# Performance work log

Measured on AMD Instinct MI355X. Metric: run time of the kernel, lower is better.

The kernel has to match this reference:

```python
import jax, jax.numpy as jnp
import numpy as np

EMBED_DIM = 512
Q_DIM = 64
V_DIM = 64
WINDOW_SIZE = 128
B, N = 2, 4096


def setup_inputs() -> dict:
    key = jax.random.key(0)
    ks = jax.random.split(key, 7)
    s = 1.0 / np.sqrt(EMBED_DIM)
    u = lambda k, shape: jax.random.uniform(k, shape, jnp.float32, -s, s)
    return {
        "x": jax.random.normal(ks[0], (B, N, EMBED_DIM), jnp.float32),
        "Wq": u(ks[1], (EMBED_DIM, Q_DIM)),
        "bq": u(ks[2], (Q_DIM,)),
        "Wk": u(ks[3], (EMBED_DIM, Q_DIM)),
        "bk": u(ks[4], (Q_DIM,)),
        "Wv": u(ks[5], (EMBED_DIM, V_DIM)),
        "bv": u(ks[6], (V_DIM,)),
    }


def reference(x, Wq, bq, Wk, bk, Wv, bv):
    b, n, _ = x.shape
    w = WINDOW_SIZE // 2
    Q = x @ Wq + bq  # (b, n, Qd)
    K = x @ Wk + bk  # (b, n, Qd)
    V = x @ Wv + bv  # (b, n, Vd)

    diags = jnp.arange(-w, w + 1)            # (nd,) offsets di
    nd = diags.shape[0]
    # Gather K[i + di] via padded K; invalid positions masked to 0 afterwards.
    Kpad = jnp.pad(K, ((0, 0), (w, w), (0, 0)))
    j = jnp.arange(n)[:, None] + diags[None, :]          # (n, nd) = i + di
    Kg = Kpad[:, j + w, :]                               # (b, n, nd, Qd)
    scores = jnp.einsum('bnd,bnod->bno', Q, Kg)          # (b, n, nd)
    valid = (j >= 0) & (j < n)
    scores = jnp.where(valid[None], scores, 0.0)

    # Faithful to original: diagonal dot products are scattered into the FIRST
    # nd columns of a dense (b, n, n) matrix (rest zeros), softmax over the
    # full n columns, then dense matmul with V.
    columns = jnp.zeros((b, n, n), dtype=x.dtype).at[:, :, :nd].set(scores)
    attn = jax.nn.softmax(columns, axis=2)               # (b, n, n)
    return attn @ V                                      # (b, n, Vd)
```

## Files before the change

### kernel.cpp

```cpp
#include <hip/hip_runtime.h>

typedef short short8 __attribute__((ext_vector_type(8)));
typedef float f32x4 __attribute__((ext_vector_type(4)));

#define NN 4096
#define NE 512
#define HD 64
#define KROWS 4288
#define KOFF  64

__device__ __forceinline__ unsigned short bf_trunc(float f) {
    union { float f; unsigned u; } c; c.f = f;
    return (unsigned short)(c.u >> 16);
}
__device__ __forceinline__ void bf_split(float f, unsigned short& hi, unsigned short& lo) {
    union { float f; unsigned u; } c; c.f = f;
    unsigned uh = c.u & 0xFFFF0000u;
    hi = (unsigned short)(uh >> 16);
    union { float f; unsigned u; } d; d.u = uh;
    lo = bf_trunc(f - d.f);
}

#define MFMA16(a, b, c) __builtin_amdgcn_mfma_f32_16x16x32_bf16((a), (b), (c), 0, 0, 0)

__global__ __launch_bounds__(256) void wprep_kernel(
    const float* __restrict__ Wq, const float* __restrict__ Wk,
    const float* __restrict__ Wv,
    unsigned short* __restrict__ Wfhi, unsigned short* __restrict__ Wflo,
    unsigned short* __restrict__ Khi, unsigned short* __restrict__ Klo,
    unsigned short* __restrict__ Vfhi, unsigned short* __restrict__ Vflo,
    float* __restrict__ Vs)
{
    const int gtid = blockIdx.x * 256 + threadIdx.x;
    const int L = gtid & 63;
    {
        const int nt = (gtid >> 6) % 12;
        const int kt = gtid / 768;
        const int n = nt * 16 + (L & 15);
        const int kbase = kt * 32 + (L >> 4) * 8;
        const float* src; int col;
        if (n < 64)       { src = Wq; col = n; }
        else if (n < 128) { src = Wk; col = n - 64; }
        else              { src = Wv; col = n - 128; }
        short8 sh, sl;
#pragma unroll
        for (int j = 0; j < 8; ++j) {
            unsigned short h, l;
            bf_split(src[(size_t)(kbase + j) * HD + col], h, l);
            sh[j] = (short)h; sl[j] = (short)l;
        }
        *(short8*)(Wfhi + (size_t)gtid * 8) = sh;
        *(short8*)(Wflo + (size_t)gtid * 8) = sl;
    }
    if (gtid < 6144) {
        const int p = gtid >> 3, o = gtid & 7;
        const int b = p / 192, q = p - b * 192;
        const size_t row = (size_t)b * KROWS + (q < 64 ? q : 4096 + q);
        const short8 z = {0, 0, 0, 0, 0, 0, 0, 0};
        *(short8*)(Khi + row * HD + o * 8) = z;
        *(short8*)(Klo + row * HD + o * 8) = z;
    }
    if (gtid < 3200) {
        const int rem = gtid % 1600;
        const int jt = rem / 320;
        const int nt = (rem / 64) % 5;
        short8 sh = {0, 0, 0, 0, 0, 0, 0, 0};
        const short8 z = {0, 0, 0, 0, 0, 0, 0, 0};
        if (nt == 4 && (L & 15) == 0) {
#pragma unroll
            for (int jj = 0; jj < 8; ++jj) {
                const int j = jt * 32 + (L >> 4) * 8 + jj;
                if (j < 129) sh[jj] = (short)0x3F80;
            }
        }
        *(short8*)(Vfhi + (size_t)gtid * 8) = sh;
        *(short8*)(Vflo + (size_t)gtid * 8) = z;
    }
    if (gtid < 128) Vs[gtid] = 0.f;
}

__global__ __launch_bounds__(256, 2) void proj_kernel(
    const float* __restrict__ x,
    const unsigned short* __restrict__ Wfhi, const unsigned short* __restrict__ Wflo,
    const float* __restrict__ bq, const float* __restrict__ bk,
    const float* __restrict__ bv,
    unsigned short* __restrict__ Qhi, unsigned short* __restrict__ Qlo,
    unsigned short* __restrict__ Khi, unsigned short* __restrict__ Klo,
    unsigned short* __restrict__ Vfhi, unsigned short* __restrict__ Vflo,
    float* __restrict__ Vs)
{
    __shared__ float V_lds[16][68];
    const int tid = threadIdx.x;
    const int L = tid & 63;
    const int w = tid >> 6;
    const int m = L & 15, kg = L >> 4;
    const int blk = blockIdx.x;
    const int r0 = blk * 16;
    const int b = blk >> 8;

    const float* xp = x + (size_t)(r0 + m) * NE + kg * 8;
    const unsigned short* wfh = Wfhi + (size_t)(w * 3) * 512 + L * 8;
    const unsigned short* wfl = Wflo + (size_t)(w * 3) * 512 + L * 8;

    f32x4 acc[3];
#pragma unroll
    for (int t = 0; t < 3; ++t) acc[t] = (f32x4){0.f, 0.f, 0.f, 0.f};

    float4 cx0[3], cx1[3];
    short8 cwh[3][3], cwl[3][3];

#pragma unroll
    for (int p = 0; p < 2; ++p) {
        cx0[p] = *(const float4*)(xp + p * 32);
        cx1[p] = *(const float4*)(xp + p * 32 + 4);
#pragma unroll
        for (int t = 0; t < 3; ++t) {
            cwh[p][t] = *(const short8*)(wfh + (size_t)p * 6144 + t * 512);
            cwl[p][t] = *(const short8*)(wfl + (size_t)p * 6144 + t * 512);
        }
    }

#pragma unroll
    for (int kt = 0; kt < 16; ++kt) {
        const int cur = kt % 3;
        const int nxt = (kt + 2) % 3;
        if (kt + 2 < 16) {
            cx0[nxt] = *(const float4*)(xp + (kt + 2) * 32);
            cx1[nxt] = *(const float4*)(xp + (kt + 2) * 32 + 4);
#pragma unroll
            for (int t = 0; t < 3; ++t) {
                cwh[nxt][t] = *(const short8*)(wfh + (size_t)(kt + 2) * 6144 + t * 512);
                cwl[nxt][t] = *(const short8*)(wfl + (size_t)(kt + 2) * 6144 + t * 512);
            }
        }
        const float xv[8] = {cx0[cur].x, cx0[cur].y, cx0[cur].z, cx0[cur].w,
                             cx1[cur].x, cx1[cur].y, cx1[cur].z, cx1[cur].w};
        short8 ahi, alo;
#pragma unroll
        for (int j = 0; j < 8; ++j) {
            unsigned short h, l; bf_split(xv[j], h, l);
            ahi[j] = (short)h; alo[j] = (short)l;
        }
#pragma unroll
        for (int t = 0; t < 3; ++t) {
            acc[t] = MFMA16(ahi, cwh[cur][t], acc[t]);
            acc[t] = MFMA16(alo, cwh[cur][t], acc[t]);
            acc[t] = MFMA16(ahi, cwl[cur][t], acc[t]);
        }
    }

#pragma unroll
    for (int t = 0; t < 3; ++t) {
        const int nt = w * 3 + t;
        const int cgc = nt * 16 + m;
        const float bias = (cgc < 64) ? bq[cgc]
                         : (cgc < 128) ? bk[cgc - 64] : bv[cgc - 128];
#pragma unroll
        for (int r = 0; r < 4; ++r) {
            const int gr = r0 + kg * 4 + r;
            const float val = acc[t][r] + bias;
            if (cgc < 64) {
                unsigned short h, l; bf_split(val, h, l);
                Qhi[(size_t)gr * HD + cgc] = h;
                Qlo[(size_t)gr * HD + cgc] = l;
            } else if (cgc < 128) {
                const int d = cgc - 64, n = gr & 4095;
                const size_t idx = ((size_t)b * KROWS + KOFF + n) * HD + d;
                unsigned short h, l; bf_split(val, h, l);
                Khi[idx] = h; Klo[idx] = l;
            } else {
                V_lds[kg * 4 + r][cgc - 128] = val;
            }
        }
    }
    __syncthreads();

    if (tid < 64) {
        float s = 0.f;
#pragma unroll
        for (int r = 0; r < 16; ++r) s += V_lds[r][tid];
        atomicAdd(&Vs[b * HD + tid], s);
    }

    if ((blk & 255) <= 8) {
        const int n0v = r0 & 4095;
        const int jt = n0v >> 5;
        const int h = (n0v >> 4) & 1;
        if ((kg >> 1) == h) {
            const int nt = w;
            short8 sh, sl;
#pragma unroll
            for (int jj = 0; jj < 8; ++jj) {
                const int j = jt * 32 + kg * 8 + jj;
                float val = 0.f;
                if (j < 129) val = V_lds[j - n0v][nt * 16 + m];
                unsigned short hh, ll; bf_split(val, hh, ll);
                sh[jj] = (short)hh; sl[jj] = (short)ll;
            }
            const size_t fo = ((size_t)((b * 25 + jt * 5 + nt) * 64 + L)) * 8;
            *(short8*)(Vfhi + fo) = sh;
            *(short8*)(Vflo + fo) = sl;
        }
    }
}

__global__ __launch_bounds__(256) void attn_kernel(
    const unsigned short* __restrict__ Qhi, const unsigned short* __restrict__ Qlo,
    const unsigned short* __restrict__ Khi, const unsigned short* __restrict__ Klo,
    const unsigned short* __restrict__ Vfhi, const unsigned short* __restrict__ Vflo,
    const float* __restrict__ Vs, float* __restrict__ out)
{
    __shared__ __align__(16) unsigned short wt_hi[16 * 168];
    __shared__ __align__(16) unsigned short wt_lo[16 * 168];
    __shared__ float den_lds[16];

    const int tid = threadIdx.x;
    const int L = tid & 63;
    const int w = tid >> 6;
    const int m = L & 15, kg = L >> 4;
    const int b = blockIdx.x >> 8;
    const int n0 = (blockIdx.x & 255) * 16;

    const unsigned short* qp  = Qhi + ((size_t)(b * NN + n0 + m)) * HD + kg * 8;
    const unsigned short* qp2 = Qlo + ((size_t)(b * NN + n0 + m)) * HD + kg * 8;
    const short8 qhi0 = *(const short8*)(qp);
    const short8 qhi1 = *(const short8*)(qp + 32);
    const short8 qlo0 = *(const short8*)(qp2);
    const short8 qlo1 = *(const short8*)(qp2 + 32);

    int kts[3]; int nkt;
    if (w == 3) { kts[0] = 3; kts[1] = 7; kts[2] = 8; nkt = 3; }
    else        { kts[0] = w; kts[1] = w + 4; kts[2] = 0; nkt = 2; }

    const unsigned short* KB  = Khi + (size_t)b * KROWS * HD;
    const unsigned short* KB2 = Klo + (size_t)b * KROWS * HD;
    short8 kh0[3], kh1[3], kl0[3], kl1[3];
#pragma unroll
    for (int i = 0; i < 3; ++i) {
        if (i < nkt) {
            const size_t krow = (size_t)(n0 + kts[i] * 16 + m);
            const unsigned short* kp  = KB  + krow * HD + kg * 8;
            const unsigned short* kp2 = KB2 + krow * HD + kg * 8;
            kh0[i] = *(const short8*)(kp);
            kh1[i] = *(const short8*)(kp + 32);
            kl0[i] = *(const short8*)(kp2);
            kl1[i] = *(const short8*)(kp2 + 32);
        }
    }

    short8 vhi[5], vlo[5], vh4[5];
#pragma unroll
    for (int jt = 0; jt < 5; ++jt) {
        const size_t fo = ((size_t)((b * 25 + jt * 5 + w) * 64 + L)) * 8;
        vhi[jt] = *(const short8*)(Vfhi + fo);
        vlo[jt] = *(const short8*)(Vflo + fo);
    }
    if (w == 0) {
#pragma unroll
        for (int jt = 0; jt < 5; ++jt) {
            const size_t fo4 = ((size_t)((b * 25 + jt * 5 + 4) * 64 + L)) * 8;
            vh4[jt] = *(const short8*)(Vfhi + fo4);
        }
    }

    for (int i = tid; i < (16 * 168) / 2; i += 256) {
        ((int*)wt_hi)[i] = 0;
        ((int*)wt_lo)[i] = 0;
    }
    __syncthreads();

#pragma unroll
    for (int i = 0; i < 3; ++i) {
        if (i < nkt) {
            f32x4 acc = (f32x4){0.f, 0.f, 0.f, 0.f};
            acc = MFMA16(qhi0, kh0[i], acc);
            acc = MFMA16(qhi1, kh1[i], acc);
            acc = MFMA16(qlo0, kh0[i], acc);
            acc = MFMA16(qlo1, kh1[i], acc);
            acc = MFMA16(qhi0, kl0[i], acc);
            acc = MFMA16(qhi1, kl1[i], acc);
            const int l = kts[i] * 16 + m;
#pragma unroll
            for (int r = 0; r < 4; ++r) {
                const int q = kg * 4 + r;
                const int j = l - q;
                if (j >= 0 && j < 129) {
                    const float wval = __expf(acc[r]) - 1.0f;
                    unsigned short h, lo2; bf_split(wval, h, lo2);
                    wt_hi[q * 168 + j] = h;
                    wt_lo[q * 168 + j] = lo2;
                }
            }
        }
    }
    __syncthreads();

    f32x4 oacc = (f32x4){0.f, 0.f, 0.f, 0.f};
    f32x4 dacc = (f32x4){0.f, 0.f, 0.f, 0.f};
#pragma unroll
    for (int jt = 0; jt < 5; ++jt) {
        const short8 whi = *(const short8*)(wt_hi + m * 168 + jt * 32 + kg * 8);
        const short8 wlo = *(const short8*)(wt_lo + m * 168 + jt * 32 + kg * 8);
        oacc = MFMA16(whi, vhi[jt], oacc);
        oacc = MFMA16(wlo, vhi[jt], oacc);
        oacc = MFMA16(whi, vlo[jt], oacc);
        if (w == 0) {
            dacc = MFMA16(whi, vh4[jt], dacc);
            dacc = MFMA16(wlo, vh4[jt], dacc);
        }
    }
    if (w == 0 && m == 0) {
#pragma unroll
        for (int r = 0; r < 4; ++r) den_lds[kg * 4 + r] = dacc[r];
    }
    __syncthreads();

    {
        const float vs = Vs[b * HD + w * 16 + m];
#pragma unroll
        for (int r = 0; r < 4; ++r) {
            const int q = kg * 4 + r;
            const float val = (vs + oacc[r]) / (4096.f + den_lds[q]);
            out[((size_t)(b * NN + n0 + q)) * HD + w * 16 + m] = val;
        }
    }
}

extern "C" void kernel_launch(void* const* d_in, const int* in_sizes, int n_in,
                              void* d_out, int out_size, void* d_ws, size_t ws_size,
                              hipStream_t stream)
{
    const float* x  = (const float*)d_in[0];
    const float* Wq = (const float*)d_in[1];
    const float* bq = (const float*)d_in[2];
    const float* Wk = (const float*)d_in[3];
    const float* bk = (const float*)d_in[4];
    const float* Wv = (const float*)d_in[5];
    const float* bv = (const float*)d_in[6];
    float* out = (float*)d_out;

    char* ws = (char*)d_ws;
    float*          Vs   = (float*)(ws + 0);
    unsigned short* Khi  = (unsigned short*)(ws + 512);
    unsigned short* Klo  = (unsigned short*)(ws + 1098240);
    unsigned short* Qhi  = (unsigned short*)(ws + 2195968);
    unsigned short* Qlo  = (unsigned short*)(ws + 3244544);
    unsigned short* Wfhi = (unsigned short*)(ws + 4359168);
    unsigned short* Wflo = (unsigned short*)(ws + 4555776);
    unsigned short* Vfhi = (unsigned short*)(ws + 4752384);
    unsigned short* Vflo = (unsigned short*)(ws + 4803584);

    wprep_kernel<<<48, 256, 0, stream>>>(Wq, Wk, Wv, Wfhi, Wflo,
                                         Khi, Klo, Vfhi, Vflo, Vs);
    proj_kernel<<<512, 256, 0, stream>>>(x, Wfhi, Wflo, bq, bk, bv,
                                         Qhi, Qlo, Khi, Klo, Vfhi, Vflo, Vs);
    attn_kernel<<<512, 256, 0, stream>>>(Qhi, Qlo, Khi, Klo, Vfhi, Vflo, Vs, out);
}
```

Measured before the change: 104.6 us.

## Restructure projection kernel into 64-row blocks of 512 threads

The projection kernel now uses 128 blocks of 512 threads, each covering 64 rows, instead of 512 blocks of 256 threads covering 16 rows. Each wave computes 6 of the 12 output column tiles for a 16-row slab, and the triple-buffered prefetch becomes double-buffered. The intent is to raise weight reuse per block and cut the number of Vs atomics. The Vf fragment writes are reworked to fit the new row mapping. With only 128 blocks, the grid may underfill a 256-CU device, and the added per-thread registers could lower occupancy.

After: 119.1 us. 13.9% more time.

```diff
diff --git a/kernel.cpp b/kernel.cpp
--- a/kernel.cpp
+++ b/kernel.cpp
@@ -79,7 +79,7 @@
     if (gtid < 128) Vs[gtid] = 0.f;
 }
 
-__global__ __launch_bounds__(256, 2) void proj_kernel(
+__global__ __launch_bounds__(512) void proj_kernel(
     const float* __restrict__ x,
     const unsigned short* __restrict__ Wfhi, const unsigned short* __restrict__ Wflo,
     const float* __restrict__ bq, const float* __restrict__ bk,
@@ -89,52 +89,47 @@
     unsigned short* __restrict__ Vfhi, unsigned short* __restrict__ Vflo,
     float* __restrict__ Vs)
 {
-    __shared__ float V_lds[16][68];
+    __shared__ float V_lds[64][68];
     const int tid = threadIdx.x;
     const int L = tid & 63;
     const int w = tid >> 6;
     const int m = L & 15, kg = L >> 4;
     const int blk = blockIdx.x;
-    const int r0 = blk * 16;
-    const int b = blk >> 8;
-
-    const float* xp = x + (size_t)(r0 + m) * NE + kg * 8;
-    const unsigned short* wfh = Wfhi + (size_t)(w * 3) * 512 + L * 8;
-    const unsigned short* wfl = Wflo + (size_t)(w * 3) * 512 + L * 8;
-
-    f32x4 acc[3];
-#pragma unroll
-    for (int t = 0; t < 3; ++t) acc[t] = (f32x4){0.f, 0.f, 0.f, 0.f};
-
-    float4 cx0[3], cx1[3];
-    short8 cwh[3][3], cwl[3][3];
-
-#pragma unroll
-    for (int p = 0; p < 2; ++p) {
-        cx0[p] = *(const float4*)(xp + p * 32);
-        cx1[p] = *(const float4*)(xp + p * 32 + 4);
-#pragma unroll
-        for (int t = 0; t < 3; ++t) {
-            cwh[p][t] = *(const short8*)(wfh + (size_t)p * 6144 + t * 512);
-            cwl[p][t] = *(const short8*)(wfl + (size_t)p * 6144 + t * 512);
-        }
+    const int r0 = blk * 64;
+    const int b = blk >> 6;
+    const int rowbase = r0 + (w >> 1) * 16;
+    const int ch = (w & 1) * 6;
+
+    const float* xp = x + (size_t)(rowbase + m) * NE + kg * 8;
+
+    f32x4 acc[6];
+#pragma unroll
+    for (int t = 0; t < 6; ++t) acc[t] = (f32x4){0.f, 0.f, 0.f, 0.f};
+
+    float4 xa0 = *(const float4*)(xp);
+    float4 xa1 = *(const float4*)(xp + 4);
+    short8 wh[6], wl[6];
+#pragma unroll
+    for (int t = 0; t < 6; ++t) {
+        wh[t] = *(const short8*)(Wfhi + (size_t)(ch + t) * 512 + L * 8);
+        wl[t] = *(const short8*)(Wflo + (size_t)(ch + t) * 512 + L * 8);
     }
 
 #pragma unroll
     for (int kt = 0; kt < 16; ++kt) {
-        const int cur = kt % 3;
-        const int nxt = (kt + 2) % 3;
-        if (kt + 2 < 16) {
-            cx0[nxt] = *(const float4*)(xp + (kt + 2) * 32);
-            cx1[nxt] = *(const float4*)(xp + (kt + 2) * 32 + 4);
-#pragma unroll
-            for (int t = 0; t < 3; ++t) {
-                cwh[nxt][t] = *(const short8*)(wfh + (size_t)(kt + 2) * 6144 + t * 512);
-                cwl[nxt][t] = *(const short8*)(wfl + (size_t)(kt + 2) * 6144 + t * 512);
-            }
-        }
-        const float xv[8] = {cx0[cur].x, cx0[cur].y, cx0[cur].z, cx0[cur].w,
-                             cx1[cur].x, cx1[cur].y, cx1[cur].z, cx1[cur].w};
+        float4 xb0, xb1;
+        short8 nh[6], nl[6];
+        if (kt < 15) {
+            xb0 = *(const float4*)(xp + (kt + 1) * 32);
+            xb1 = *(const float4*)(xp + (kt + 1) * 32 + 4);
+#pragma unroll
+            for (int t = 0; t < 6; ++t) {
+                nh[t] = *(const short8*)(Wfhi + (size_t)((kt + 1) * 12 + ch + t) * 512 + L * 8);
+                nl[t] = *(const short8*)(Wflo + (size_t)((kt + 1) * 12 + ch + t) * 512 + L * 8);
+            }
+        }
+        const float xv[8] = {xa0.x, xa0.y, xa0.z, xa0.w,
+                             xa1.x, xa1.y, xa1.z, xa1.w};
         short8 ahi, alo;
 #pragma unroll
         for (int j = 0; j < 8; ++j) {
@@ -142,22 +137,27 @@
             ahi[j] = (short)h; alo[j] = (short)l;
         }
 #pragma unroll
-        for (int t = 0; t < 3; ++t) {
-            acc[t] = MFMA16(ahi, cwh[cur][t], acc[t]);
-            acc[t] = MFMA16(alo, cwh[cur][t], acc[t]);
-            acc[t] = MFMA16(ahi, cwl[cur][t], acc[t]);
-        }
-    }
-
-#pragma unroll
-    for (int t = 0; t < 3; ++t) {
-        const int nt = w * 3 + t;
+        for (int t = 0; t < 6; ++t) {
+            acc[t] = MFMA16(ahi, wh[t], acc[t]);
+            acc[t] = MFMA16(alo, wh[t], acc[t]);
+            acc[t] = MFMA16(ahi, wl[t], acc[t]);
+        }
+        if (kt < 15) {
+            xa0 = xb0; xa1 = xb1;
+#pragma unroll
+            for (int t = 0; t < 6; ++t) { wh[t] = nh[t]; wl[t] = nl[t]; }
+        }
+    }
+
+#pragma unroll
+    for (int t = 0; t < 6; ++t) {
+        const int nt = ch + t;
         const int cgc = nt * 16 + m;
         const float bias = (cgc < 64) ? bq[cgc]
                          : (cgc < 128) ? bk[cgc - 64] : bv[cgc - 128];
 #pragma unroll
         for (int r = 0; r < 4; ++r) {
-            const int gr = r0 + kg * 4 + r;
+            const int gr = rowbase + kg * 4 + r;
             const float val = acc[t][r] + bias;
             if (cgc < 64) {
                 unsigned short h, l; bf_split(val, h, l);
@@ -169,7 +169,7 @@
                 unsigned short h, l; bf_split(val, h, l);
                 Khi[idx] = h; Klo[idx] = l;
             } else {
-                V_lds[kg * 4 + r][cgc - 128] = val;
+                V_lds[(w >> 1) * 16 + kg * 4 + r][cgc - 128] = val;
             }
         }
     }
@@ -178,26 +178,36 @@
     if (tid < 64) {
         float s = 0.f;
 #pragma unroll
-        for (int r = 0; r < 16; ++r) s += V_lds[r][tid];
+        for (int r = 0; r < 64; ++r) s += V_lds[r][tid];
         atomicAdd(&Vs[b * HD + tid], s);
     }
 
-    if ((blk & 255) <= 8) {
-        const int n0v = r0 & 4095;
-        const int jt = n0v >> 5;
-        const int h = (n0v >> 4) & 1;
-        if ((kg >> 1) == h) {
+    {
+        const int local = blk & 63;
+        if (local < 2) {
+            const int jt = local * 2 + (w >> 2);
+            const int nt = w & 3;
+            short8 sh, sl;
+#pragma unroll
+            for (int jj = 0; jj < 8; ++jj) {
+                const int lrow = (w >> 2) * 32 + kg * 8 + jj;
+                unsigned short hh, ll;
+                bf_split(V_lds[lrow][nt * 16 + m], hh, ll);
+                sh[jj] = (short)hh; sl[jj] = (short)ll;
+            }
+            const size_t fo = ((size_t)((b * 25 + jt * 5 + nt) * 64 + L)) * 8;
+            *(short8*)(Vfhi + fo) = sh;
+            *(short8*)(Vflo + fo) = sl;
+        } else if (local == 2 && w < 4) {
             const int nt = w;
-            short8 sh, sl;
-#pragma unroll
-            for (int jj = 0; jj < 8; ++jj) {
-                const int j = jt * 32 + kg * 8 + jj;
-                float val = 0.f;
-                if (j < 129) val = V_lds[j - n0v][nt * 16 + m];
-                unsigned short hh, ll; bf_split(val, hh, ll);
-                sh[jj] = (short)hh; sl[jj] = (short)ll;
-            }
-            const size_t fo = ((size_t)((b * 25 + jt * 5 + nt) * 64 + L)) * 8;
+            short8 sh = {0, 0, 0, 0, 0, 0, 0, 0};
+            short8 sl = {0, 0, 0, 0, 0, 0, 0, 0};
+            if (kg == 0) {
+                unsigned short hh, ll;
+                bf_split(V_lds[0][nt * 16 + m], hh, ll);
+                sh[0] = (short)hh; sl[0] = (short)ll;
+            }
+            const size_t fo = ((size_t)((b * 25 + 4 * 5 + nt) * 64 + L)) * 8;
             *(short8*)(Vfhi + fo) = sh;
             *(short8*)(Vflo + fo) = sl;
         }
@@ -352,7 +362,7 @@
 
     wprep_kernel<<<48, 256, 0, stream>>>(Wq, Wk, Wv, Wfhi, Wflo,
                                          Khi, Klo, Vfhi, Vflo, Vs);
-    proj_kernel<<<512, 256, 0, stream>>>(x, Wfhi, Wflo, bq, bk, bv,
+    proj_kernel<<<128, 512, 0, stream>>>(x, Wfhi, Wflo, bq, bk, bv,
                                          Qhi, Qlo, Khi, Klo, Vfhi, Vflo, Vs);
     attn_kernel<<<512, 256, 0, stream>>>(Qhi, Qlo, Khi, Klo, Vfhi, Vflo, Vs, out);
 }
```

## Switch split-bf16 MFMA emulation to fp16 with fewer correction terms

Applied to the files above, without the earlier changes.

Replaces the bf16 hi/lo split arithmetic with fp16 (hi/lo for activations only), dropping the low parts of weights, K and V. This removes a third of the MFMAs and halves several workspace buffers and loads. The attention weights are scaled by 1/256 to stay within fp16 range, and the scale is undone at the end. The projection kernel now runs 512-thread blocks that split K across two halves and reduce the partial sums through LDS. Accuracy is lower because fp16 has a narrower range and only one operand is split.

After: 98.07 us (median of 2 runs). 6.2% less time.

```diff
diff --git a/kernel.cpp b/kernel.cpp
--- a/kernel.cpp
+++ b/kernel.cpp
@@ -1,6 +1,6 @@
 #include <hip/hip_runtime.h>
 
-typedef short short8 __attribute__((ext_vector_type(8)));
+typedef _Float16 half8 __attribute__((ext_vector_type(8)));
 typedef float f32x4 __attribute__((ext_vector_type(4)));
 
 #define NN 4096
@@ -8,28 +8,20 @@
 #define HD 64
 #define KROWS 4288
 #define KOFF  64
-
-__device__ __forceinline__ unsigned short bf_trunc(float f) {
-    union { float f; unsigned u; } c; c.f = f;
-    return (unsigned short)(c.u >> 16);
-}
-__device__ __forceinline__ void bf_split(float f, unsigned short& hi, unsigned short& lo) {
-    union { float f; unsigned u; } c; c.f = f;
-    unsigned uh = c.u & 0xFFFF0000u;
-    hi = (unsigned short)(uh >> 16);
-    union { float f; unsigned u; } d; d.u = uh;
-    lo = bf_trunc(f - d.f);
-}
-
-#define MFMA16(a, b, c) __builtin_amdgcn_mfma_f32_16x16x32_bf16((a), (b), (c), 0, 0, 0)
+#define WSCALE (1.0f / 256.0f)
+
+__device__ __forceinline__ void f16_split(float f, _Float16& hi, _Float16& lo) {
+    hi = (_Float16)f;
+    lo = (_Float16)(f - (float)hi);
+}
+
+#define MFMA16(a, b, c) __builtin_amdgcn_mfma_f32_16x16x32_f16((a), (b), (c), 0, 0, 0)
 
 __global__ __launch_bounds__(256) void wprep_kernel(
     const float* __restrict__ Wq, const float* __restrict__ Wk,
     const float* __restrict__ Wv,
-    unsigned short* __restrict__ Wfhi, unsigned short* __restrict__ Wflo,
-    unsigned short* __restrict__ Khi, unsigned short* __restrict__ Klo,
-    unsigned short* __restrict__ Vfhi, unsigned short* __restrict__ Vflo,
-    float* __restrict__ Vs)
+    _Float16* __restrict__ Wf, _Float16* __restrict__ Khi,
+    _Float16* __restrict__ Vf, float* __restrict__ Vs)
 {
     const int gtid = blockIdx.x * 256 + threadIdx.x;
     const int L = gtid & 63;
@@ -42,53 +34,45 @@
         if (n < 64)       { src = Wq; col = n; }
         else if (n < 128) { src = Wk; col = n - 64; }
         else              { src = Wv; col = n - 128; }
-        short8 sh, sl;
-#pragma unroll
-        for (int j = 0; j < 8; ++j) {
-            unsigned short h, l;
-            bf_split(src[(size_t)(kbase + j) * HD + col], h, l);
-            sh[j] = (short)h; sl[j] = (short)l;
-        }
-        *(short8*)(Wfhi + (size_t)gtid * 8) = sh;
-        *(short8*)(Wflo + (size_t)gtid * 8) = sl;
+        half8 sh;
+#pragma unroll
+        for (int j = 0; j < 8; ++j)
+            sh[j] = (_Float16)src[(size_t)(kbase + j) * HD + col];
+        *(half8*)(Wf + (size_t)gtid * 8) = sh;
     }
     if (gtid < 6144) {
         const int p = gtid >> 3, o = gtid & 7;
         const int b = p / 192, q = p - b * 192;
         const size_t row = (size_t)b * KROWS + (q < 64 ? q : 4096 + q);
-        const short8 z = {0, 0, 0, 0, 0, 0, 0, 0};
-        *(short8*)(Khi + row * HD + o * 8) = z;
-        *(short8*)(Klo + row * HD + o * 8) = z;
+        const half8 z = {0, 0, 0, 0, 0, 0, 0, 0};
+        *(half8*)(Khi + row * HD + o * 8) = z;
     }
     if (gtid < 3200) {
         const int rem = gtid % 1600;
         const int jt = rem / 320;
         const int nt = (rem / 64) % 5;
-        short8 sh = {0, 0, 0, 0, 0, 0, 0, 0};
-        const short8 z = {0, 0, 0, 0, 0, 0, 0, 0};
+        half8 sh = {0, 0, 0, 0, 0, 0, 0, 0};
         if (nt == 4 && (L & 15) == 0) {
 #pragma unroll
             for (int jj = 0; jj < 8; ++jj) {
                 const int j = jt * 32 + (L >> 4) * 8 + jj;
-                if (j < 129) sh[jj] = (short)0x3F80;
+                if (j < 129) sh[jj] = (_Float16)1.0f;
             }
         }
-        *(short8*)(Vfhi + (size_t)gtid * 8) = sh;
-        *(short8*)(Vflo + (size_t)gtid * 8) = z;
+        *(half8*)(Vf + (size_t)gtid * 8) = sh;
     }
     if (gtid < 128) Vs[gtid] = 0.f;
 }
 
-__global__ __launch_bounds__(256, 2) void proj_kernel(
-    const float* __restrict__ x,
-    const unsigned short* __restrict__ Wfhi, const unsigned short* __restrict__ Wflo,
+__global__ __launch_bounds__(512) void proj_kernel(
+    const float* __restrict__ x, const _Float16* __restrict__ Wf,
     const float* __restrict__ bq, const float* __restrict__ bk,
     const float* __restrict__ bv,
-    unsigned short* __restrict__ Qhi, unsigned short* __restrict__ Qlo,
-    unsigned short* __restrict__ Khi, unsigned short* __restrict__ Klo,
-    unsigned short* __restrict__ Vfhi, unsigned short* __restrict__ Vflo,
+    _Float16* __restrict__ Qhi, _Float16* __restrict__ Qlo,
+    _Float16* __restrict__ Khi, _Float16* __restrict__ Vf,
     float* __restrict__ Vs)
 {
+    __shared__ float parts[4][3][64][4];
     __shared__ float V_lds[16][68];
     const int tid = threadIdx.x;
     const int L = tid & 63;
@@ -97,79 +81,65 @@
     const int blk = blockIdx.x;
     const int r0 = blk * 16;
     const int b = blk >> 8;
-
-    const float* xp = x + (size_t)(r0 + m) * NE + kg * 8;
-    const unsigned short* wfh = Wfhi + (size_t)(w * 3) * 512 + L * 8;
-    const unsigned short* wfl = Wflo + (size_t)(w * 3) * 512 + L * 8;
+    const int t3 = w & 3;
+    const int h = w >> 2;
+
+    const float* xp = x + (size_t)(r0 + m) * NE + h * 256 + kg * 8;
+    const _Float16* wfb = Wf + ((size_t)(h * 8) * 12 + t3 * 3) * 512 + L * 8;
 
     f32x4 acc[3];
 #pragma unroll
     for (int t = 0; t < 3; ++t) acc[t] = (f32x4){0.f, 0.f, 0.f, 0.f};
 
-    float4 cx0[3], cx1[3];
-    short8 cwh[3][3], cwl[3][3];
-
-#pragma unroll
-    for (int p = 0; p < 2; ++p) {
-        cx0[p] = *(const float4*)(xp + p * 32);
-        cx1[p] = *(const float4*)(xp + p * 32 + 4);
+#pragma unroll
+    for (int kt = 0; kt < 8; ++kt) {
+        const float4 x0 = *(const float4*)(xp + kt * 32);
+        const float4 x1 = *(const float4*)(xp + kt * 32 + 4);
+        const float xv[8] = {x0.x, x0.y, x0.z, x0.w, x1.x, x1.y, x1.z, x1.w};
+        half8 ahi, alo;
+#pragma unroll
+        for (int j = 0; j < 8; ++j) {
+            _Float16 hh, ll; f16_split(xv[j], hh, ll);
+            ahi[j] = hh; alo[j] = ll;
+        }
 #pragma unroll
         for (int t = 0; t < 3; ++t) {
-            cwh[p][t] = *(const short8*)(wfh + (size_t)p * 6144 + t * 512);
-            cwl[p][t] = *(const short8*)(wfl + (size_t)p * 6144 + t * 512);
-        }
-    }
-
-#pragma unroll
-    for (int kt = 0; kt < 16; ++kt) {
-        const int cur = kt % 3;
-        const int nxt = (kt + 2) % 3;
-        if (kt + 2 < 16) {
-            cx0[nxt] = *(const float4*)(xp + (kt + 2) * 32);
-            cx1[nxt] = *(const float4*)(xp + (kt + 2) * 32 + 4);
-#pragma unroll
-            for (int t = 0; t < 3; ++t) {
-                cwh[nxt][t] = *(const short8*)(wfh + (size_t)(kt + 2) * 6144 + t * 512);
-                cwl[nxt][t] = *(const short8*)(wfl + (size_t)(kt + 2) * 6144 + t * 512);
-            }
-        }
-        const float xv[8] = {cx0[cur].x, cx0[cur].y, cx0[cur].z, cx0[cur].w,
-                             cx1[cur].x, cx1[cur].y, cx1[cur].z, cx1[cur].w};
-        short8 ahi, alo;
-#pragma unroll
-        for (int j = 0; j < 8; ++j) {
-            unsigned short h, l; bf_split(xv[j], h, l);
-            ahi[j] = (short)h; alo[j] = (short)l;
-        }
+            const half8 wv = *(const half8*)(wfb + (size_t)kt * 6144 + t * 512);
+            acc[t] = MFMA16(ahi, wv, acc[t]);
+            acc[t] = MFMA16(alo, wv, acc[t]);
+        }
+    }
+
+    if (h == 1) {
+#pragma unroll
+        for (int t = 0; t < 3; ++t)
+            *(f32x4*)(&parts[t3][t][L][0]) = acc[t];
+    }
+    __syncthreads();
+
+    if (h == 0) {
 #pragma unroll
         for (int t = 0; t < 3; ++t) {
-            acc[t] = MFMA16(ahi, cwh[cur][t], acc[t]);
-            acc[t] = MFMA16(alo, cwh[cur][t], acc[t]);
-            acc[t] = MFMA16(ahi, cwl[cur][t], acc[t]);
-        }
-    }
-
-#pragma unroll
-    for (int t = 0; t < 3; ++t) {
-        const int nt = w * 3 + t;
-        const int cgc = nt * 16 + m;
-        const float bias = (cgc < 64) ? bq[cgc]
-                         : (cgc < 128) ? bk[cgc - 64] : bv[cgc - 128];
-#pragma unroll
-        for (int r = 0; r < 4; ++r) {
-            const int gr = r0 + kg * 4 + r;
-            const float val = acc[t][r] + bias;
-            if (cgc < 64) {
-                unsigned short h, l; bf_split(val, h, l);
-                Qhi[(size_t)gr * HD + cgc] = h;
-                Qlo[(size_t)gr * HD + cgc] = l;
-            } else if (cgc < 128) {
-                const int d = cgc - 64, n = gr & 4095;
-                const size_t idx = ((size_t)b * KROWS + KOFF + n) * HD + d;
-                unsigned short h, l; bf_split(val, h, l);
-                Khi[idx] = h; Klo[idx] = l;
-            } else {
-                V_lds[kg * 4 + r][cgc - 128] = val;
+            const f32x4 p = *(const f32x4*)(&parts[t3][t][L][0]);
+            acc[t] += p;
+            const int nt = t3 * 3 + t;
+            const int cgc = nt * 16 + m;
+            const float bias = (cgc < 64) ? bq[cgc]
+                             : (cgc < 128) ? bk[cgc - 64] : bv[cgc - 128];
+#pragma unroll
+            for (int r = 0; r < 4; ++r) {
+                const int gr = r0 + kg * 4 + r;
+                const float val = acc[t][r] + bias;
+                if (cgc < 64) {
+                    _Float16 hh, ll; f16_split(val, hh, ll);
+                    Qhi[(size_t)gr * HD + cgc] = hh;
+                    Qlo[(size_t)gr * HD + cgc] = ll;
+                } else if (cgc < 128) {
+                    const int d = cgc - 64, n = gr & 4095;
+                    Khi[((size_t)b * KROWS + KOFF + n) * HD + d] = (_Float16)val;
+                } else {
+                    V_lds[kg * 4 + r][cgc - 128] = val;
+                }
             }
         }
     }
@@ -182,36 +152,38 @@
         atomicAdd(&Vs[b * HD + tid], s);
     }
 
-    if ((blk & 255) <= 8) {
-        const int n0v = r0 & 4095;
-        const int jt = n0v >> 5;
-        const int h = (n0v >> 4) & 1;
-        if ((kg >> 1) == h) {
+    {
+        const int local = blk & 255;
+        if (local < 8 && w < 4) {
+            const int jt = local >> 1;
+            if ((kg >> 1) == (local & 1)) {
+                const int nt = w;
+                half8 sh;
+#pragma unroll
+                for (int jj = 0; jj < 8; ++jj) {
+                    const int lrow = (kg - (local & 1) * 2) * 8 + jj;
+                    sh[jj] = (_Float16)V_lds[lrow][nt * 16 + m];
+                }
+                const size_t fo = ((size_t)((b * 25 + jt * 5 + nt) * 64 + L)) * 8;
+                *(half8*)(Vf + fo) = sh;
+            }
+        } else if (local == 8 && w < 4 && kg == 0) {
             const int nt = w;
-            short8 sh, sl;
-#pragma unroll
-            for (int jj = 0; jj < 8; ++jj) {
-                const int j = jt * 32 + kg * 8 + jj;
-                float val = 0.f;
-                if (j < 129) val = V_lds[j - n0v][nt * 16 + m];
-                unsigned short hh, ll; bf_split(val, hh, ll);
-                sh[jj] = (short)hh; sl[jj] = (short)ll;
-            }
-            const size_t fo = ((size_t)((b * 25 + jt * 5 + nt) * 64 + L)) * 8;
-            *(short8*)(Vfhi + fo) = sh;
-            *(short8*)(Vflo + fo) = sl;
+            half8 sh = {0, 0, 0, 0, 0, 0, 0, 0};
+            sh[0] = (_Float16)V_lds[0][nt * 16 + m];
+            const size_t fo = ((size_t)((b * 25 + 4 * 5 + nt) * 64 + L)) * 8;
+            *(half8*)(Vf + fo) = sh;
         }
     }
 }
 
 __global__ __launch_bounds__(256) void attn_kernel(
-    const unsigned short* __restrict__ Qhi, const unsigned short* __restrict__ Qlo,
-    const unsigned short* __restrict__ Khi, const unsigned short* __restrict__ Klo,
-    const unsigned short* __restrict__ Vfhi, const unsigned short* __restrict__ Vflo,
+    const _Float16* __restrict__ Qhi, const _Float16* __restrict__ Qlo,
+    const _Float16* __restrict__ Khi, const _Float16* __restrict__ Vf,
     const float* __restrict__ Vs, float* __restrict__ out)
 {
-    __shared__ __align__(16) unsigned short wt_hi[16 * 168];
-    __shared__ __align__(16) unsigned short wt_lo[16 * 168];
+    __shared__ __align__(16) _Float16 wt_hi[16 * 168];
+    __shared__ __align__(16) _Float16 wt_lo[16 * 168];
     __shared__ float den_lds[16];
 
     const int tid = threadIdx.x;
@@ -221,45 +193,39 @@
     const int b = blockIdx.x >> 8;
     const int n0 = (blockIdx.x & 255) * 16;
 
-    const unsigned short* qp  = Qhi + ((size_t)(b * NN + n0 + m)) * HD + kg * 8;
-    const unsigned short* qp2 = Qlo + ((size_t)(b * NN + n0 + m)) * HD + kg * 8;
-    const short8 qhi0 = *(const short8*)(qp);
-    const short8 qhi1 = *(const short8*)(qp + 32);
-    const short8 qlo0 = *(const short8*)(qp2);
-    const short8 qlo1 = *(const short8*)(qp2 + 32);
+    const _Float16* qp  = Qhi + ((size_t)(b * NN + n0 + m)) * HD + kg * 8;
+    const _Float16* qp2 = Qlo + ((size_t)(b * NN + n0 + m)) * HD + kg * 8;
+    const half8 qhi0 = *(const half8*)(qp);
+    const half8 qhi1 = *(const half8*)(qp + 32);
+    const half8 qlo0 = *(const half8*)(qp2);
+    const half8 qlo1 = *(const half8*)(qp2 + 32);
 
     int kts[3]; int nkt;
     if (w == 3) { kts[0] = 3; kts[1] = 7; kts[2] = 8; nkt = 3; }
     else        { kts[0] = w; kts[1] = w + 4; kts[2] = 0; nkt = 2; }
 
-    const unsigned short* KB  = Khi + (size_t)b * KROWS * HD;
-    const unsigned short* KB2 = Klo + (size_t)b * KROWS * HD;
-    short8 kh0[3], kh1[3], kl0[3], kl1[3];
+    const _Float16* KB = Khi + (size_t)b * KROWS * HD;
+    half8 kh0[3], kh1[3];
 #pragma unroll
     for (int i = 0; i < 3; ++i) {
         if (i < nkt) {
-            const size_t krow = (size_t)(n0 + kts[i] * 16 + m);
-            const unsigned short* kp  = KB  + krow * HD + kg * 8;
-            const unsigned short* kp2 = KB2 + krow * HD + kg * 8;
-            kh0[i] = *(const short8*)(kp);
-            kh1[i] = *(const short8*)(kp + 32);
-            kl0[i] = *(const short8*)(kp2);
-            kl1[i] = *(const short8*)(kp2 + 32);
-        }
-    }
-
-    short8 vhi[5], vlo[5], vh4[5];
+            const _Float16* kp = KB + (size_t)(n0 + kts[i] * 16 + m) * HD + kg * 8;
+            kh0[i] = *(const half8*)(kp);
+            kh1[i] = *(const half8*)(kp + 32);
+        }
+    }
+
+    half8 vhi[5], vh4[5];
 #pragma unroll
     for (int jt = 0; jt < 5; ++jt) {
         const size_t fo = ((size_t)((b * 25 + jt * 5 + w) * 64 + L)) * 8;
-        vhi[jt] = *(const short8*)(Vfhi + fo);
-        vlo[jt] = *(const short8*)(Vflo + fo);
+        vhi[jt] = *(const half8*)(Vf + fo);
     }
     if (w == 0) {
 #pragma unroll
         for (int jt = 0; jt < 5; ++jt) {
             const size_t fo4 = ((size_t)((b * 25 + jt * 5 + 4) * 64 + L)) * 8;
-            vh4[jt] = *(const short8*)(Vfhi + fo4);
+            vh4[jt] = *(const half8*)(Vf + fo4);
         }
     }
 
@@ -277,18 +243,16 @@
             acc = MFMA16(qhi1, kh1[i], acc);
             acc = MFMA16(qlo0, kh0[i], acc);
             acc = MFMA16(qlo1, kh1[i], acc);
-            acc = MFMA16(qhi0, kl0[i], acc);
-            acc = MFMA16(qhi1, kl1[i], acc);
             const int l = kts[i] * 16 + m;
 #pragma unroll
             for (int r = 0; r < 4; ++r) {
                 const int q = kg * 4 + r;
                 const int j = l - q;
                 if (j >= 0 && j < 129) {
-                    const float wval = __expf(acc[r]) - 1.0f;
-                    unsigned short h, lo2; bf_split(wval, h, lo2);
-                    wt_hi[q * 168 + j] = h;
-                    wt_lo[q * 168 + j] = lo2;
+                    const float wval = (__expf(acc[r]) - 1.0f) * WSCALE;
+                    _Float16 hh, ll; f16_split(wval, hh, ll);
+                    wt_hi[q * 168 + j] = hh;
+                    wt_lo[q * 168 + j] = ll;
                 }
             }
         }
@@ -299,11 +263,10 @@
     f32x4 dacc = (f32x4){0.f, 0.f, 0.f, 0.f};
 #pragma unroll
     for (int jt = 0; jt < 5; ++jt) {
-        const short8 whi = *(const short8*)(wt_hi + m * 168 + jt * 32 + kg * 8);
-        const short8 wlo = *(const short8*)(wt_lo + m * 168 + jt * 32 + kg * 8);
+        const half8 whi = *(const half8*)(wt_hi + m * 168 + jt * 32 + kg * 8);
+        const half8 wlo = *(const half8*)(wt_lo + m * 168 + jt * 32 + kg * 8);
         oacc = MFMA16(whi, vhi[jt], oacc);
         oacc = MFMA16(wlo, vhi[jt], oacc);
-        oacc = MFMA16(whi, vlo[jt], oacc);
         if (w == 0) {
             dacc = MFMA16(whi, vh4[jt], dacc);
             dacc = MFMA16(wlo, vh4[jt], dacc);
@@ -320,7 +283,8 @@
 #pragma unroll
         for (int r = 0; r < 4; ++r) {
             const int q = kg * 4 + r;
-            const float val = (vs + oacc[r]) / (4096.f + den_lds[q]);
+            const float val = (vs + 256.0f * oacc[r])
+                            / (4096.f + 256.0f * den_lds[q]);
             out[((size_t)(b * NN + n0 + q)) * HD + w * 16 + m] = val;
         }
     }
@@ -340,19 +304,15 @@
     float* out = (float*)d_out;
 
     char* ws = (char*)d_ws;
-    float*          Vs   = (float*)(ws + 0);
-    unsigned short* Khi  = (unsigned short*)(ws + 512);
-    unsigned short* Klo  = (unsigned short*)(ws + 1098240);
-    unsigned short* Qhi  = (unsigned short*)(ws + 2195968);
-    unsigned short* Qlo  = (unsigned short*)(ws + 3244544);
-    unsigned short* Wfhi = (unsigned short*)(ws + 4359168);
-    unsigned short* Wflo = (unsigned short*)(ws + 4555776);
-    unsigned short* Vfhi = (unsigned short*)(ws + 4752384);
-    unsigned short* Vflo = (unsigned short*)(ws + 4803584);
-
-    wprep_kernel<<<48, 256, 0, stream>>>(Wq, Wk, Wv, Wfhi, Wflo,
-                                         Khi, Klo, Vfhi, Vflo, Vs);
-    proj_kernel<<<512, 256, 0, stream>>>(x, Wfhi, Wflo, bq, bk, bv,
-                                         Qhi, Qlo, Khi, Klo, Vfhi, Vflo, Vs);
-    attn_kernel<<<512, 256, 0, stream>>>(Qhi, Qlo, Khi, Klo, Vfhi, Vflo, Vs, out);
-}
+    float*     Vs  = (float*)(ws + 0);
+    _Float16*  Khi = (_Float16*)(ws + 512);
+    _Float16*  Qhi = (_Float16*)(ws + 1098240);
+    _Float16*  Qlo = (_Float16*)(ws + 2146816);
+    _Float16*  Wf  = (_Float16*)(ws + 3195392);
+    _Float16*  Vf  = (_Float16*)(ws + 3392000);
+
+    wprep_kernel<<<48, 256, 0, stream>>>(Wq, Wk, Wv, Wf, Khi, Vf, Vs);
+    proj_kernel<<<512, 512, 0, stream>>>(x, Wf, bq, bk, bv,
+                                         Qhi, Qlo, Khi, Vf, Vs);
+    attn_kernel<<<512, 256, 0, stream>>>(Qhi, Qlo, Khi, Vf, Vs, out);
+}
```
